# Kernel optimization log

Measured on AMD Instinct MI355X. Metric: run time of the kernel, lower is better.

Reference implementation:

```python
import jax, jax.numpy as jnp
import numpy as np

B, S_ENC, S_DEC = 4, 2048, 1024
ENC_DIM, DEC_DIM, H = 1024, 1024, 16
CROSS_DIM = max(ENC_DIM, DEC_DIM)
HEAD_DIM_DEC = DEC_DIM // H
SCALE = HEAD_DIM_DEC ** 0.5  # module divides by dec_scaling only


def _linear_params(key, d_in, d_out):
    kw, kb = jax.random.split(key)
    bound = 1.0 / np.sqrt(d_in)
    W = jax.random.uniform(kw, (d_in, d_out), jnp.float32, -bound, bound)
    b = jax.random.uniform(kb, (d_out,), jnp.float32, -bound, bound)
    return W, b


def setup_inputs() -> dict:
    key = jax.random.key(0)
    ks = jax.random.split(key, 7)
    enc = jax.random.normal(ks[0], (B, S_ENC, ENC_DIM), jnp.float32)
    dec = jax.random.normal(ks[1], (B, S_DEC, DEC_DIM), jnp.float32)
    enc_mask = jax.random.uniform(ks[2], (B, 1, 1, S_ENC)) < 0.1
    q_w, q_b = _linear_params(ks[3], DEC_DIM, CROSS_DIM)
    k_w, k_b = _linear_params(ks[4], ENC_DIM, CROSS_DIM)
    v_w, v_b = _linear_params(ks[5], ENC_DIM, DEC_DIM)
    o_w, o_b = _linear_params(ks[6], DEC_DIM, DEC_DIM)
    return {"enc": enc, "enc_mask": enc_mask, "dec": dec,
            "q_w": q_w, "q_b": q_b, "k_w": k_w, "k_b": k_b,
            "v_w": v_w, "v_b": v_b, "o_w": o_w, "o_b": o_b}


def _split_heads(x):
    b, s, d = x.shape
    return x.reshape(b, s, H, d // H).transpose(0, 2, 1, 3)  # [b,h,s,hd]


def reference(enc, enc_mask, dec, q_w, q_b, k_w, k_b, v_w, v_b, o_w, o_b):
    q = _split_heads(dec @ q_w + q_b)   # [B,H,Sq,cross_hd]
    k = _split_heads(enc @ k_w + k_b)   # [B,H,Sk,cross_hd]
    v = _split_heads(enc @ v_w + v_b)   # [B,H,Sk,dec_hd]
    logits = jnp.einsum('bhqd,bhkd->bhqk', q, k) / SCALE
    logits = jnp.where(enc_mask, -jnp.inf, logits)
    a = jax.nn.softmax(logits, axis=-1)
    x = jnp.einsum('bhqk,bhkd->bhqd', a, v)          # [B,H,Sq,dec_hd]
    x = x.transpose(0, 2, 1, 3).reshape(x.shape[0], x.shape[2], -1)  # [B,Sq,DEC_DIM]
    return x @ o_w + o_b
```

## Files before the change

kernel.cpp:

```cpp
#include <hip/hip_runtime.h>
#include <hip/hip_bf16.h>
#include <cstdint>

#define BB   4
#define SENC 2048
#define SDEC 1024
#define DM   1024
#define NH   16
#define HD   64

using short8 = __attribute__((ext_vector_type(8))) short;
using f32x4  = __attribute__((ext_vector_type(4))) float;

__device__ inline unsigned short f2bf(float f) {
    return (unsigned short)((__builtin_bit_cast(unsigned int, f) + 0x8000u) >> 16);
}
__device__ inline unsigned int pk2bf(float a, float b) {
    return ((__builtin_bit_cast(unsigned int, a) + 0x8000u) >> 16) |
           ((__builtin_bit_cast(unsigned int, b) + 0x8000u) & 0xffff0000u);
}

__device__ inline float fexp2(float x) {
#if __has_builtin(__builtin_amdgcn_exp2f)
    return __builtin_amdgcn_exp2f(x);
#else
    return exp2f(x);
#endif
}

__device__ inline size_t frag_off(int m, int k) {
    return (size_t)(m >> 4) * 16384 + (size_t)(k >> 3) * 128 + ((m & 15) << 3) + (k & 7);
}

__global__ __launch_bounds__(256) void prep_kernel(
    const float* __restrict__ dec, const float* __restrict__ enc,
    unsigned short* __restrict__ decb, unsigned short* __restrict__ encb,
    const float* __restrict__ qw, const float* __restrict__ kw,
    const float* __restrict__ vw, const float* __restrict__ ow,
    unsigned short* __restrict__ qwt, unsigned short* __restrict__ kvwt,
    unsigned short* __restrict__ owt,
    const int* __restrict__ mask, float* __restrict__ maskf) {
    const int id = blockIdx.x, tid = threadIdx.x;
    if (id < 3072) {
        __shared__ unsigned short t[64][72];
        const int rt = id >> 4, ct = id & 15, k0 = ct * 64;
        const float* src; unsigned short* dst; int m0;
        if (rt < 64) { src = dec; dst = decb; m0 = rt * 64; }
        else         { src = enc; dst = encb; m0 = (rt - 64) * 64; }
        #pragma unroll
        for (int i = 0; i < 4; ++i) {
            const int row = i * 16 + (tid >> 4), col4 = (tid & 15) * 4;
            float4 v = *(const float4*)&src[(size_t)(m0 + row) * DM + k0 + col4];
            ushort4 o;
            o.x = f2bf(v.x); o.y = f2bf(v.y); o.z = f2bf(v.z); o.w = f2bf(v.w);
            *(ushort4*)&t[row][col4] = o;
        }
        __syncthreads();
        const int f = tid >> 3, sub = tid & 7;
        const int mt = f >> 3, kc = f & 7;
        const int row0 = mt * 16 + sub * 2;
        short8 a = *(const short8*)&t[row0][kc * 8];
        short8 b = *(const short8*)&t[row0 + 1][kc * 8];
        size_t off = (size_t)(m0 / 16 + mt) * 16384 + (size_t)(k0 / 8 + kc) * 128 + sub * 16;
        *(short8*)&dst[off] = a;
        *(short8*)&dst[off + 8] = b;
        return;
    }
    if (id == 4096) {
        for (int j = tid; j < BB * SENC; j += 256) maskf[j] = mask[j] ? -1e30f : 0.0f;
        return;
    }
    __shared__ float t[64][65];
    const int id2 = id - 3072;
    const int z = id2 >> 8, ky = (id2 >> 4) & 15, nx = id2 & 15;
    const float* src; unsigned short* dst;
    switch (z) {
        case 0:  src = qw; dst = qwt; break;
        case 1:  src = kw; dst = kvwt; break;
        case 2:  src = vw; dst = kvwt + (size_t)64 * 16384; break;
        default: src = ow; dst = owt; break;
    }
    const int k0 = ky * 64, n0 = nx * 64;
    #pragma unroll
    for (int it = 0; it < 16; ++it) {
        int e = it * 256 + tid, r = e >> 6, c = e & 63;
        t[r][c] = src[(size_t)(k0 + r) * DM + n0 + c];
    }
    __syncthreads();
    #pragma unroll
    for (int it = 0; it < 16; ++it) {
        int e = it * 256 + tid, r = e >> 6, c = e & 63;
        size_t off = (size_t)((n0 + r) >> 4) * 16384 + (size_t)((k0 + c) >> 3) * 128
                   + ((r & 15) << 3) + (c & 7);
        dst[off] = f2bf(t[c][r]);
    }
}

__global__ __launch_bounds__(256) void gemm_qkv_kernel(
    const unsigned short* __restrict__ encb, const unsigned short* __restrict__ decb,
    const unsigned short* __restrict__ kvwt, const unsigned short* __restrict__ qwt,
    const float* __restrict__ q_b, const float* __restrict__ k_b, const float* __restrict__ v_b,
    unsigned short* __restrict__ Qb, unsigned short* __restrict__ Kb,
    unsigned short* __restrict__ Vtb) {
    const int id = blockIdx.x;
    const bool isKV = id < 1024;
    const unsigned short *A, *Bw;
    int m0, n0;
    if (isKV) {
        const int x = id & 7, w = id >> 3;
        A = encb; Bw = kvwt;
        m0 = (x * 8 + (w >> 4)) * 128;
        n0 = (w & 15) * 128;
    } else {
        const int i2 = id - 1024, x = i2 & 7, w = i2 >> 3;
        A = decb; Bw = qwt;
        m0 = (x * 4 + (w >> 3)) * 128;
        n0 = (w & 7) * 128;
    }
    const int tid = threadIdx.x;
    const int wave = tid >> 6, lane = tid & 63, quad = lane >> 4, l16 = lane & 15;
    const int wr = wave >> 1, wc = wave & 1;
    const int lo = quad * 128 + l16 * 8;
    const unsigned short* Ap = A + (size_t)(m0 / 16 + wr * 4) * 16384 + lo;
    const unsigned short* Bp = Bw + (size_t)(n0 / 16 + wc * 4) * 16384 + lo;
    f32x4 acc[4][4] = {};
    short8 ac[4], bc[4], an[4], bn[4];
    #pragma unroll
    for (int i = 0; i < 4; ++i) {
        ac[i] = *(const short8*)&Ap[i * 16384];
        bc[i] = *(const short8*)&Bp[i * 16384];
    }
    #pragma unroll 2
    for (int it = 0; it < 32; ++it) {
        if (it < 31) {
            const int ko = (it + 1) * 512;
            #pragma unroll
            for (int i = 0; i < 4; ++i) {
                an[i] = *(const short8*)&Ap[i * 16384 + ko];
                bn[i] = *(const short8*)&Bp[i * 16384 + ko];
            }
        }
        #pragma unroll
        for (int i = 0; i < 4; ++i)
            #pragma unroll
            for (int j = 0; j < 4; ++j)
                acc[i][j] = __builtin_amdgcn_mfma_f32_16x16x32_bf16(ac[i], bc[j], acc[i][j], 0, 0, 0);
        #pragma unroll
        for (int i = 0; i < 4; ++i) { ac[i] = an[i]; bc[i] = bn[i]; }
    }
    #pragma unroll
    for (int i = 0; i < 4; ++i) {
        #pragma unroll
        for (int j = 0; j < 4; ++j) {
            const int gc = n0 + wc * 64 + j * 16 + l16;
            const int gr0 = m0 + wr * 64 + i * 16 + quad * 4;
            if (!isKV) {
                const float bv = q_b[gc];
                const int h = gc >> 6, d = gc & 63;
                #pragma unroll
                for (int rr = 0; rr < 4; ++rr) {
                    int gr = gr0 + rr, b = gr >> 10, sq = gr & 1023;
                    float v = (acc[i][j][rr] + bv) * 0.18033688011112042f;
                    Qb[(((size_t)(b * NH + h) * SDEC + sq) << 6) + d] = f2bf(v);
                }
            } else if (gc < 1024) {
                const float bv = k_b[gc];
                const int h = gc >> 6, d = gc & 63;
                #pragma unroll
                for (int rr = 0; rr < 4; ++rr) {
                    int gr = gr0 + rr, b = gr >> 11, sk = gr & 2047;
                    size_t off = (size_t)(b * NH + h) * 131072 + (size_t)(sk >> 4) * 1024
                               + ((d >> 3) << 7) + ((sk & 15) << 3) + (d & 7);
                    Kb[off] = f2bf(acc[i][j][rr] + bv);
                }
            } else {
                const int gc2 = gc & 1023;
                const float bv = v_b[gc2];
                const int h = gc2 >> 6, d = gc2 & 63;
                const int b = gr0 >> 11, sk0 = gr0 & 2047;
                size_t off = (size_t)(b * NH + h) * 131072 + (size_t)(d >> 4) * 32768
                           + (size_t)(sk0 >> 3) * 128 + ((d & 15) << 3) + (sk0 & 7);
                uint2 pk;
                pk.x = pk2bf(acc[i][j][0] + bv, acc[i][j][1] + bv);
                pk.y = pk2bf(acc[i][j][2] + bv, acc[i][j][3] + bv);
                *(uint2*)&Vtb[off] = pk;
            }
        }
    }
}

__global__ __launch_bounds__(256) void gemm_o_kernel(const unsigned short* __restrict__ A,
                                                     const unsigned short* __restrict__ Bw,
                                                     const float* __restrict__ bias,
                                                     float* __restrict__ Cout) {
    const int id = blockIdx.x, x = id & 7, w = id >> 3;
    const int m0 = (x * 8 + (w >> 3)) * 64, n0 = (w & 7) * 128;
    const int tid = threadIdx.x;
    const int wave = tid >> 6, lane = tid & 63, quad = lane >> 4, l16 = lane & 15;
    const int lo = quad * 128 + l16 * 8;
    const unsigned short* Ap = A + (size_t)(m0 / 16) * 16384 + lo;
    const unsigned short* Bp = Bw + (size_t)(n0 / 16 + wave * 2) * 16384 + lo;
    f32x4 acc[4][2] = {};
    short8 ac[4], bc[2], an[4], bn[2];
    #pragma unroll
    for (int i = 0; i < 4; ++i) ac[i] = *(const short8*)&Ap[i * 16384];
    #pragma unroll
    for (int j = 0; j < 2; ++j) bc[j] = *(const short8*)&Bp[j * 16384];
    #pragma unroll 2
    for (int it = 0; it < 32; ++it) {
        if (it < 31) {
            const int ko = (it + 1) * 512;
            #pragma unroll
            for (int i = 0; i < 4; ++i) an[i] = *(const short8*)&Ap[i * 16384 + ko];
            #pragma unroll
            for (int j = 0; j < 2; ++j) bn[j] = *(const short8*)&Bp[j * 16384 + ko];
        }
        #pragma unroll
        for (int i = 0; i < 4; ++i)
            #pragma unroll
            for (int j = 0; j < 2; ++j)
                acc[i][j] = __builtin_amdgcn_mfma_f32_16x16x32_bf16(ac[i], bc[j], acc[i][j], 0, 0, 0);
        #pragma unroll
        for (int i = 0; i < 4; ++i) ac[i] = an[i];
        #pragma unroll
        for (int j = 0; j < 2; ++j) bc[j] = bn[j];
    }
    #pragma unroll
    for (int i = 0; i < 4; ++i)
        #pragma unroll
        for (int j = 0; j < 2; ++j) {
            const int gc = n0 + wave * 32 + j * 16 + l16;
            const float bv = bias[gc];
            #pragma unroll
            for (int rr = 0; rr < 4; ++rr) {
                const int gr = m0 + i * 16 + quad * 4 + rr;
                Cout[(size_t)gr * DM + gc] = acc[i][j][rr] + bv;
            }
        }
}

__global__ __launch_bounds__(256) void attn_kernel(const unsigned short* __restrict__ Qb,
                                                   const unsigned short* __restrict__ Kb,
                                                   const unsigned short* __restrict__ Vtb,
                                                   const float* __restrict__ maskf,
                                                   unsigned short* __restrict__ Xb) {
    __shared__ __align__(16) unsigned short Ps[4][16 * 72];
    const int id = blockIdx.x, x = id & 7, r = id >> 3;
    const int bh = x * 8 + (r & 7), qt = r >> 3;
    const int b = bh >> 4, h = bh & 15;
    const int q0 = qt * 64;
    const int tid = threadIdx.x, wave = tid >> 6, lane = tid & 63;
    const int quad = lane >> 4, l16 = lane & 15;
    const int lo = quad * 128 + l16 * 8;

    const unsigned short* Kfp = Kb + (size_t)bh * 131072 + lo;
    const unsigned short* Vfp = Vtb + (size_t)bh * 131072 + lo;
    const float* mp = maskf + (size_t)b * SENC;

    short8 qf0, qf1;
    {
        const unsigned short* Qp = Qb + ((size_t)bh * SDEC + q0 + wave * 16) * HD;
        qf0 = *(const short8*)&Qp[l16 * HD + quad * 8];
        qf1 = *(const short8*)&Qp[l16 * HD + 32 + quad * 8];
    }

    float lsum = 0.f;
    f32x4 o[4] = {};
    short8 kc0[4], kc1[4], kn0[4], kn1[4];
    #pragma unroll
    for (int j = 0; j < 4; ++j) {
        kc0[j] = *(const short8*)&Kfp[j * 1024];
        kc1[j] = *(const short8*)&Kfp[j * 1024 + 512];
    }

    #pragma unroll 2
    for (int it = 0; it < SENC / 64; ++it) {
        const int kb = it * 64;
        short8 vB0[4], vB1[4];
        const unsigned short* vt = Vfp + (size_t)(kb >> 3) * 128;
        #pragma unroll
        for (int j = 0; j < 4; ++j) {
            vB0[j] = *(const short8*)&vt[j * 32768];
            vB1[j] = *(const short8*)&vt[j * 32768 + 512];
        }
        float4 mf[4];
        #pragma unroll
        for (int j = 0; j < 4; ++j) mf[j] = *(const float4*)&mp[kb + j * 16 + quad * 4];
        f32x4 st[4];
        #pragma unroll
        for (int j = 0; j < 4; ++j) {
            f32x4 z = {0.f, 0.f, 0.f, 0.f};
            z = __builtin_amdgcn_mfma_f32_16x16x32_bf16(kc0[j], qf0, z, 0, 0, 0);
            st[j] = __builtin_amdgcn_mfma_f32_16x16x32_bf16(kc1[j], qf1, z, 0, 0, 0);
        }
        if (it + 1 < SENC / 64) {
            const unsigned short* kt = Kfp + (size_t)((it + 1) * 4) * 1024;
            #pragma unroll
            for (int j = 0; j < 4; ++j) {
                kn0[j] = *(const short8*)&kt[j * 1024];
                kn1[j] = *(const short8*)&kt[j * 1024 + 512];
            }
        }
        #pragma unroll
        for (int j = 0; j < 4; ++j) {
            float p0 = fexp2(st[j][0] + mf[j].x);
            float p1 = fexp2(st[j][1] + mf[j].y);
            float p2 = fexp2(st[j][2] + mf[j].z);
            float p3 = fexp2(st[j][3] + mf[j].w);
            lsum += (p0 + p1) + (p2 + p3);
            uint2 pkv;
            pkv.x = pk2bf(p0, p1);
            pkv.y = pk2bf(p2, p3);
            *(uint2*)&Ps[wave][l16 * 72 + j * 16 + quad * 4] = pkv;
        }
        asm volatile("s_waitcnt lgkmcnt(0)" ::: "memory");
        short8 pA0 = *(const short8*)&Ps[wave][l16 * 72 + quad * 8];
        short8 pA1 = *(const short8*)&Ps[wave][l16 * 72 + 32 + quad * 8];
        #pragma unroll
        for (int dj = 0; dj < 4; ++dj) {
            o[dj] = __builtin_amdgcn_mfma_f32_16x16x32_bf16(pA0, vB0[dj], o[dj], 0, 0, 0);
            o[dj] = __builtin_amdgcn_mfma_f32_16x16x32_bf16(pA1, vB1[dj], o[dj], 0, 0, 0);
        }
        #pragma unroll
        for (int j = 0; j < 4; ++j) { kc0[j] = kn0[j]; kc1[j] = kn1[j]; }
    }
    lsum += __shfl_xor(lsum, 16);
    lsum += __shfl_xor(lsum, 32);
    const int mtile = b * 64 + qt * 4 + wave;
    const int kbase = h * 64;
    #pragma unroll
    for (int rr = 0; rr < 4; ++rr) {
        float iv = 1.0f / __shfl(lsum, quad * 4 + rr, 64);
        #pragma unroll
        for (int dj = 0; dj < 4; ++dj) {
            const int k = kbase + dj * 16 + l16;
            size_t off = (size_t)mtile * 16384 + (size_t)(k >> 3) * 128
                       + ((quad * 4 + rr) << 3) + (k & 7);
            Xb[off] = f2bf(o[dj][rr] * iv);
        }
    }
}

extern "C" void kernel_launch(void* const* d_in, const int* in_sizes, int n_in,
                              void* d_out, int out_size, void* d_ws, size_t ws_size,
                              hipStream_t stream) {
    const float* enc   = (const float*)d_in[0];
    const int*   emask = (const int*)d_in[1];
    const float* dec   = (const float*)d_in[2];
    const float* q_w   = (const float*)d_in[3];
    const float* q_b   = (const float*)d_in[4];
    const float* k_w   = (const float*)d_in[5];
    const float* k_b   = (const float*)d_in[6];
    const float* v_w   = (const float*)d_in[7];
    const float* v_b   = (const float*)d_in[8];
    const float* o_w   = (const float*)d_in[9];
    const float* o_b   = (const float*)d_in[10];
    float* out = (float*)d_out;

    char* ws = (char*)d_ws;
    unsigned short* decb = (unsigned short*)ws; ws += (size_t)4096 * 1024 * 2;
    unsigned short* encb = (unsigned short*)ws; ws += (size_t)8192 * 1024 * 2;
    unsigned short* qwt  = (unsigned short*)ws; ws += (size_t)1024 * 1024 * 2;
    unsigned short* kvwt = (unsigned short*)ws; ws += (size_t)2048 * 1024 * 2;
    unsigned short* owt  = (unsigned short*)ws; ws += (size_t)1024 * 1024 * 2;
    unsigned short* Qb   = (unsigned short*)ws; ws += (size_t)BB * NH * SDEC * HD * 2;
    unsigned short* Kb   = (unsigned short*)ws; ws += (size_t)BB * NH * SENC * HD * 2;
    unsigned short* Vtb  = (unsigned short*)ws; ws += (size_t)BB * NH * HD * SENC * 2;
    unsigned short* Xb   = (unsigned short*)ws; ws += (size_t)4096 * 1024 * 2;
    float*          mkf  = (float*)ws;          ws += (size_t)BB * SENC * 4;

    prep_kernel<<<4097, 256, 0, stream>>>(dec, enc, decb, encb, q_w, k_w, v_w, o_w,
                                          qwt, kvwt, owt, emask, mkf);
    gemm_qkv_kernel<<<1280, 256, 0, stream>>>(encb, decb, kvwt, qwt, q_b, k_b, v_b, Qb, Kb, Vtb);
    attn_kernel<<<1024, 256, 0, stream>>>(Qb, Kb, Vtb, mkf, Xb);
    gemm_o_kernel<<<512, 256, 0, stream>>>(Xb, owt, o_b, out);
}
```

Measured before the change: 272.3 us.

## Split attention over keys across wave pairs and reuse K/V fragments for two query groups

The attention kernel now uses 512-thread blocks covering 128 queries. Each wave handles 32 queries (two 16-row groups) so every loaded K/V fragment feeds twice as many MFMAs. The 2048 keys are split between two wave halves, whose partial outputs and row sums are combined through shared memory before normalization. This halves the per-query K/V global traffic and doubles the work per block. In exchange it drops the explicit K prefetch, raises register pressure from the doubled accumulators, and adds a block-wide sync plus extra LDS use.

```diff
diff --git a/kernel.cpp b/kernel.cpp
--- a/kernel.cpp
+++ b/kernel.cpp
@@ -26,10 +26,6 @@
 #else
     return exp2f(x);
 #endif
-}
-
-__device__ inline size_t frag_off(int m, int k) {
-    return (size_t)(m >> 4) * 16384 + (size_t)(k >> 3) * 128 + ((m & 15) << 3) + (k & 7);
 }
 
 __global__ __launch_bounds__(256) void prep_kernel(
@@ -239,43 +235,52 @@
         }
 }
 
-__global__ __launch_bounds__(256) void attn_kernel(const unsigned short* __restrict__ Qb,
-                                                   const unsigned short* __restrict__ Kb,
-                                                   const unsigned short* __restrict__ Vtb,
-                                                   const float* __restrict__ maskf,
-                                                   unsigned short* __restrict__ Xb) {
-    __shared__ __align__(16) unsigned short Ps[4][16 * 72];
+__global__ __launch_bounds__(512, 4) void attn_kernel(const unsigned short* __restrict__ Qb,
+                                                      const unsigned short* __restrict__ Kb,
+                                                      const unsigned short* __restrict__ Vtb,
+                                                      const float* __restrict__ maskf,
+                                                      unsigned short* __restrict__ Xb) {
+    __shared__ __align__(16) unsigned short Ps[8][16 * 72];
+    __shared__ __align__(16) float Sm[4][2176];
     const int id = blockIdx.x, x = id & 7, r = id >> 3;
     const int bh = x * 8 + (r & 7), qt = r >> 3;
     const int b = bh >> 4, h = bh & 15;
-    const int q0 = qt * 64;
+    const int q0 = qt * 128;
     const int tid = threadIdx.x, wave = tid >> 6, lane = tid & 63;
+    const int qw = wave & 3, ks = wave >> 2;
     const int quad = lane >> 4, l16 = lane & 15;
     const int lo = quad * 128 + l16 * 8;
 
-    const unsigned short* Kfp = Kb + (size_t)bh * 131072 + lo;
-    const unsigned short* Vfp = Vtb + (size_t)bh * 131072 + lo;
-    const float* mp = maskf + (size_t)b * SENC;
-
-    short8 qf0, qf1;
+    const unsigned short* Kfp = Kb + (size_t)bh * 131072 + (size_t)ks * 65536 + lo;
+    const unsigned short* Vfp = Vtb + (size_t)bh * 131072 + (size_t)ks * 16384 + lo;
+    const float* mp = maskf + (size_t)b * SENC + ks * 1024;
+
+    short8 qf[2][2];
     {
-        const unsigned short* Qp = Qb + ((size_t)bh * SDEC + q0 + wave * 16) * HD;
-        qf0 = *(const short8*)&Qp[l16 * HD + quad * 8];
-        qf1 = *(const short8*)&Qp[l16 * HD + 32 + quad * 8];
-    }
-
-    float lsum = 0.f;
-    f32x4 o[4] = {};
-    short8 kc0[4], kc1[4], kn0[4], kn1[4];
-    #pragma unroll
-    for (int j = 0; j < 4; ++j) {
-        kc0[j] = *(const short8*)&Kfp[j * 1024];
-        kc1[j] = *(const short8*)&Kfp[j * 1024 + 512];
-    }
+        const unsigned short* Qp = Qb + ((size_t)bh * SDEC + q0 + qw * 32) * HD;
+        #pragma unroll
+        for (int g = 0; g < 2; ++g) {
+            qf[g][0] = *(const short8*)&Qp[(g * 16 + l16) * HD + quad * 8];
+            qf[g][1] = *(const short8*)&Qp[(g * 16 + l16) * HD + 32 + quad * 8];
+        }
+    }
+
+    float lsum[2] = {0.f, 0.f};
+    f32x4 o[2][4] = {};
 
     #pragma unroll 2
-    for (int it = 0; it < SENC / 64; ++it) {
+    for (int it = 0; it < 16; ++it) {
         const int kb = it * 64;
+        short8 kc0[4], kc1[4];
+        const unsigned short* kt = Kfp + (size_t)(kb >> 4) * 1024;
+        #pragma unroll
+        for (int j = 0; j < 4; ++j) {
+            kc0[j] = *(const short8*)&kt[j * 1024];
+            kc1[j] = *(const short8*)&kt[j * 1024 + 512];
+        }
+        float4 mf[4];
+        #pragma unroll
+        for (int j = 0; j < 4; ++j) mf[j] = *(const float4*)&mp[kb + j * 16 + quad * 4];
         short8 vB0[4], vB1[4];
         const unsigned short* vt = Vfp + (size_t)(kb >> 3) * 128;
         #pragma unroll
@@ -283,60 +288,75 @@
             vB0[j] = *(const short8*)&vt[j * 32768];
             vB1[j] = *(const short8*)&vt[j * 32768 + 512];
         }
-        float4 mf[4];
-        #pragma unroll
-        for (int j = 0; j < 4; ++j) mf[j] = *(const float4*)&mp[kb + j * 16 + quad * 4];
-        f32x4 st[4];
-        #pragma unroll
-        for (int j = 0; j < 4; ++j) {
-            f32x4 z = {0.f, 0.f, 0.f, 0.f};
-            z = __builtin_amdgcn_mfma_f32_16x16x32_bf16(kc0[j], qf0, z, 0, 0, 0);
-            st[j] = __builtin_amdgcn_mfma_f32_16x16x32_bf16(kc1[j], qf1, z, 0, 0, 0);
-        }
-        if (it + 1 < SENC / 64) {
-            const unsigned short* kt = Kfp + (size_t)((it + 1) * 4) * 1024;
+        #pragma unroll
+        for (int g = 0; g < 2; ++g) {
+            f32x4 st[4];
             #pragma unroll
             for (int j = 0; j < 4; ++j) {
-                kn0[j] = *(const short8*)&kt[j * 1024];
-                kn1[j] = *(const short8*)&kt[j * 1024 + 512];
-            }
-        }
-        #pragma unroll
-        for (int j = 0; j < 4; ++j) {
-            float p0 = fexp2(st[j][0] + mf[j].x);
-            float p1 = fexp2(st[j][1] + mf[j].y);
-            float p2 = fexp2(st[j][2] + mf[j].z);
-            float p3 = fexp2(st[j][3] + mf[j].w);
-            lsum += (p0 + p1) + (p2 + p3);
-            uint2 pkv;
-            pkv.x = pk2bf(p0, p1);
-            pkv.y = pk2bf(p2, p3);
-            *(uint2*)&Ps[wave][l16 * 72 + j * 16 + quad * 4] = pkv;
-        }
-        asm volatile("s_waitcnt lgkmcnt(0)" ::: "memory");
-        short8 pA0 = *(const short8*)&Ps[wave][l16 * 72 + quad * 8];
-        short8 pA1 = *(const short8*)&Ps[wave][l16 * 72 + 32 + quad * 8];
-        #pragma unroll
-        for (int dj = 0; dj < 4; ++dj) {
-            o[dj] = __builtin_amdgcn_mfma_f32_16x16x32_bf16(pA0, vB0[dj], o[dj], 0, 0, 0);
-            o[dj] = __builtin_amdgcn_mfma_f32_16x16x32_bf16(pA1, vB1[dj], o[dj], 0, 0, 0);
-        }
-        #pragma unroll
-        for (int j = 0; j < 4; ++j) { kc0[j] = kn0[j]; kc1[j] = kn1[j]; }
-    }
-    lsum += __shfl_xor(lsum, 16);
-    lsum += __shfl_xor(lsum, 32);
-    const int mtile = b * 64 + qt * 4 + wave;
-    const int kbase = h * 64;
-    #pragma unroll
-    for (int rr = 0; rr < 4; ++rr) {
-        float iv = 1.0f / __shfl(lsum, quad * 4 + rr, 64);
-        #pragma unroll
-        for (int dj = 0; dj < 4; ++dj) {
-            const int k = kbase + dj * 16 + l16;
-            size_t off = (size_t)mtile * 16384 + (size_t)(k >> 3) * 128
-                       + ((quad * 4 + rr) << 3) + (k & 7);
-            Xb[off] = f2bf(o[dj][rr] * iv);
+                f32x4 z = {0.f, 0.f, 0.f, 0.f};
+                z = __builtin_amdgcn_mfma_f32_16x16x32_bf16(kc0[j], qf[g][0], z, 0, 0, 0);
+                st[j] = __builtin_amdgcn_mfma_f32_16x16x32_bf16(kc1[j], qf[g][1], z, 0, 0, 0);
+            }
+            #pragma unroll
+            for (int j = 0; j < 4; ++j) {
+                float p0 = fexp2(st[j][0] + mf[j].x);
+                float p1 = fexp2(st[j][1] + mf[j].y);
+                float p2 = fexp2(st[j][2] + mf[j].z);
+                float p3 = fexp2(st[j][3] + mf[j].w);
+                lsum[g] += (p0 + p1) + (p2 + p3);
+                uint2 pkv;
+                pkv.x = pk2bf(p0, p1);
+                pkv.y = pk2bf(p2, p3);
+                *(uint2*)&Ps[wave][l16 * 72 + j * 16 + quad * 4] = pkv;
+            }
+            asm volatile("s_waitcnt lgkmcnt(0)" ::: "memory");
+            short8 pA0 = *(const short8*)&Ps[wave][l16 * 72 + quad * 8];
+            short8 pA1 = *(const short8*)&Ps[wave][l16 * 72 + 32 + quad * 8];
+            #pragma unroll
+            for (int dj = 0; dj < 4; ++dj) {
+                o[g][dj] = __builtin_amdgcn_mfma_f32_16x16x32_bf16(pA0, vB0[dj], o[g][dj], 0, 0, 0);
+                o[g][dj] = __builtin_amdgcn_mfma_f32_16x16x32_bf16(pA1, vB1[dj], o[g][dj], 0, 0, 0);
+            }
+        }
+    }
+
+    if (ks == 1) {
+        float* dst = Sm[qw];
+        #pragma unroll
+        for (int g = 0; g < 2; ++g)
+            #pragma unroll
+            for (int dj = 0; dj < 4; ++dj)
+                *(f32x4*)&dst[lane * 32 + g * 16 + dj * 4] = o[g][dj];
+        dst[2048 + lane] = lsum[0];
+        dst[2112 + lane] = lsum[1];
+    }
+    __syncthreads();
+    if (ks == 0) {
+        const float* src = Sm[qw];
+        #pragma unroll
+        for (int g = 0; g < 2; ++g) {
+            #pragma unroll
+            for (int dj = 0; dj < 4; ++dj) {
+                f32x4 p = *(const f32x4*)&src[lane * 32 + g * 16 + dj * 4];
+                o[g][dj] += p;
+            }
+            lsum[g] += src[2048 + g * 64 + lane];
+            float lg = lsum[g];
+            lg += __shfl_xor(lg, 16);
+            lg += __shfl_xor(lg, 32);
+            const int mtile = (b * 1024 + q0 + qw * 32 + g * 16) >> 4;
+            const int kbase = h * 64;
+            #pragma unroll
+            for (int rr = 0; rr < 4; ++rr) {
+                float iv = 1.0f / __shfl(lg, quad * 4 + rr, 64);
+                #pragma unroll
+                for (int dj = 0; dj < 4; ++dj) {
+                    const int k = kbase + dj * 16 + l16;
+                    size_t off = (size_t)mtile * 16384 + (size_t)(k >> 3) * 128
+                               + ((quad * 4 + rr) << 3) + (k & 7);
+                    Xb[off] = f2bf(o[g][dj][rr] * iv);
+                }
+            }
         }
     }
 }
@@ -372,6 +392,6 @@
     prep_kernel<<<4097, 256, 0, stream>>>(dec, enc, decb, encb, q_w, k_w, v_w, o_w,
                                           qwt, kvwt, owt, emask, mkf);
     gemm_qkv_kernel<<<1280, 256, 0, stream>>>(encb, decb, kvwt, qwt, q_b, k_b, v_b, Qb, Kb, Vtb);
-    attn_kernel<<<1024, 256, 0, stream>>>(Qb, Kb, Vtb, mkf, Xb);
+    attn_kernel<<<512, 512, 0, stream>>>(Qb, Kb, Vtb, mkf, Xb);
     gemm_o_kernel<<<512, 256, 0, stream>>>(Xb, owt, o_b, out);
 }
```

Result: slower. 361.3 us (+32.7%).
